# Optimization experiments

Measured on AMD Instinct MI355X. Metric: run time of the kernel, lower is better.

Reference implementation:

```python
import jax, jax.numpy as jnp
import numpy as np

B, I, M, R, C = 2048, 16, 4, 4096, 10  # batch, input_dim, num_mfs, num_rules, num_classes


def setup_inputs() -> dict:
    key = jax.random.key(0)
    k1, k2, k3, k4, k5 = jax.random.split(key, 5)
    x = jax.random.normal(k1, (B, I), dtype=jnp.float32)
    centers = jax.random.normal(k2, (I, M), dtype=jnp.float32)
    widths = jax.random.uniform(k3, (I, M), dtype=jnp.float32, minval=0.5, maxval=1.5)
    consequents = jax.random.normal(k4, (R, I + 1, C), dtype=jnp.float32)
    rule_idx = jax.random.randint(k5, (I, R), 0, M, dtype=jnp.int32)
    return {"x": x, "centers": centers, "widths": widths,
            "consequents": consequents, "rule_idx": rule_idx}


def reference(x, centers, widths, consequents, rule_idx):
    # Gaussian membership functions: [B, I, M] (note: +1e-9 inside exp, as in source)
    mfs = jnp.exp(-(x[:, :, None] - centers[None]) ** 2 / (2.0 * widths[None] ** 2) + 1e-9)
    # Gather per-rule MF values along the M axis: [B, I, R]
    rule_mfs = mfs[:, jnp.arange(I)[:, None], rule_idx]
    # Product t-norm over input dims -> firing strengths [B, R]
    firing = jnp.prod(rule_mfs, axis=1)
    norm_fs = firing / (jnp.sum(firing, axis=1, keepdims=True) + 1e-9)
    # Extended input with bias [B, I+1]
    x_ext = jnp.concatenate([x, jnp.ones((x.shape[0], 1), dtype=x.dtype)], axis=1)
    # Outer product phi [B, R, I+1], then flat GEMM with consequents
    phi = norm_fs[:, :, None] * jax.lax.stop_gradient(x_ext)[:, None, :]
    y_hat = phi.reshape(x.shape[0], R * (I + 1)) @ consequents.reshape(R * (I + 1), C)
    return y_hat, norm_fs, x_ext
```

## Files before the change

kernel.cpp:

```cpp
#include <hip/hip_runtime.h>
#include <stdint.h>

typedef short short8 __attribute__((ext_vector_type(8)));
typedef float f32x4 __attribute__((ext_vector_type(4)));

#define B_ 2048
#define I_ 16
#define M_ 4
#define R_ 4096
#define C_ 10
#define NX 17
#define NW 170
#define NPAD 192
#define KSPLIT 32
#define KCH (R_ / KSPLIT)

#define Y_OFF    0
#define NORM_OFF (B_ * C_)
#define XE_OFF   (B_ * C_ + B_ * R_)

#define PK_OFF    0
#define WT_OFF    16384
#define NFB_OFF   (WT_OFF + NPAD * R_ * 2)
#define PARTY_OFF (NFB_OFF + B_ * R_ * 2)

#define MFMA16(a, b, c) __builtin_amdgcn_mfma_f32_16x16x32_bf16(a, b, c, 0, 0, 0)

__device__ __forceinline__ uint16_t f2bf(float f) {
    uint32_t u = __builtin_bit_cast(uint32_t, f);
    uint32_t r = u + 0x7fffu + ((u >> 16) & 1u);
    return (uint16_t)(r >> 16);
}

__global__ __launch_bounds__(256) void prep_kernel(
        const int* __restrict__ rule_idx, const float* __restrict__ cons,
        uint32_t* __restrict__ packed, uint16_t* __restrict__ wt) {
    int t = threadIdx.x;
    if (blockIdx.x == 64) {
        for (int r = t; r < R_; r += 256) {
            uint32_t p = 0;
#pragma unroll
            for (int i = 0; i < I_; ++i)
                p |= ((uint32_t)rule_idx[i * R_ + r] & 3u) << (2 * i);
            packed[r] = p;
        }
        return;
    }
    __shared__ float lt[64][NW + 1];
    int k0 = blockIdx.x * 64;
    for (int idx = t; idx < 64 * NW; idx += 256) {
        int k = idx / NW, n = idx - k * NW;
        lt[k][n] = cons[(size_t)(k0 + k) * NW + n];
    }
    __syncthreads();
    for (int idx = t; idx < NPAD * 32; idx += 256) {
        int n = idx >> 5, kp = idx & 31;
        uint32_t v = 0;
        if (n < NW) {
            uint32_t v0 = f2bf(lt[kp * 2][n]);
            uint32_t v1 = f2bf(lt[kp * 2 + 1][n]);
            v = v0 | (v1 << 16);
        }
        *(uint32_t*)(wt + (size_t)n * R_ + k0 + kp * 2) = v;
    }
}

__global__ __launch_bounds__(256) void fuzz_kernel(
        const float* __restrict__ x, const float* __restrict__ centers,
        const float* __restrict__ widths, const uint32_t* __restrict__ packed,
        float* __restrict__ out, uint16_t* __restrict__ nfb) {
    int b = blockIdx.x;
    int t = threadIdx.x;
    __shared__ float xs[I_];
    __shared__ float zl[64];
    __shared__ float tab4[4 * 256];
    __shared__ float wsum[4];

    if (t < I_) xs[t] = x[b * I_ + t];
    if (t < NX) out[XE_OFF + b * NX + t] = (t < I_) ? x[b * I_ + t] : 1.0f;
    __syncthreads();

    if (t < 64) {
        int i = t >> 2, m = t & 3;
        float d = xs[i] - centers[i * M_ + m];
        float w = widths[i * M_ + m];
        zl[t] = -(d * d) / (2.0f * w * w) + 1e-9f;
    }
    __syncthreads();

#pragma unroll
    for (int u = 0; u < 4; ++u) {
        int idx = t + u * 256;
        int q = idx >> 8, xq = idx & 255;
        tab4[idx] = zl[q * 16 +      (xq & 3)]
                  + zl[q * 16 +  4 + ((xq >> 2) & 3)]
                  + zl[q * 16 +  8 + ((xq >> 4) & 3)]
                  + zl[q * 16 + 12 + ((xq >> 6) & 3)];
    }
    __syncthreads();

    float fs[16];
    float lsum = 0.f;
#pragma unroll
    for (int k = 0; k < 16; ++k) {
        uint32_t p = packed[t + k * 256];
        float s = tab4[        p         & 255]
                + tab4[256 + ((p >>  8) & 255)]
                + tab4[512 + ((p >> 16) & 255)]
                + tab4[768 + ((p >> 24) & 255)];
        float f = __expf(s);
        fs[k] = f;
        lsum += f;
    }
#pragma unroll
    for (int off = 32; off > 0; off >>= 1) lsum += __shfl_down(lsum, off);
    if ((t & 63) == 0) wsum[t >> 6] = lsum;
    __syncthreads();
    float inv = 1.0f / (wsum[0] + wsum[1] + wsum[2] + wsum[3] + 1e-9f);
#pragma unroll
    for (int k = 0; k < 16; ++k) {
        float v = fs[k] * inv;
        out[NORM_OFF + (size_t)b * R_ + t + k * 256] = v;
        nfb[(size_t)b * R_ + t + k * 256] = f2bf(v);
    }
}

__global__ __launch_bounds__(256, 3) void gemm_kernel(
        const uint16_t* __restrict__ nfb,
        const uint16_t* __restrict__ wt,
        const float* __restrict__ xe,
        float* __restrict__ party) {
    int bt  = blockIdx.x;
    int ks  = blockIdx.y;
    int tid = threadIdx.x;
    int wid = tid >> 6;
    int lane = tid & 63;
    int b0 = bt * 64;
    int k0 = ks * KCH;
    int row = lane & 15;
    int kf  = (lane >> 4) * 8;

    f32x4 acc[4][3];
#pragma unroll
    for (int mt = 0; mt < 4; ++mt)
#pragma unroll
        for (int nt = 0; nt < 3; ++nt) acc[mt][nt] = (f32x4){0.f, 0.f, 0.f, 0.f};

    const uint16_t* Ab = nfb + (size_t)(b0 + row) * R_ + k0 + kf;
    const uint16_t* Bb = wt  + (size_t)(wid * 48 + row) * R_ + k0 + kf;

    short8 a[2][4], w[2][3];
#define LOADS(buf, kk)                                                   \
    do {                                                                 \
        a[buf][0] = *(const short8*)(Ab + (kk));                         \
        a[buf][1] = *(const short8*)(Ab + (size_t)16 * R_ + (kk));       \
        a[buf][2] = *(const short8*)(Ab + (size_t)32 * R_ + (kk));       \
        a[buf][3] = *(const short8*)(Ab + (size_t)48 * R_ + (kk));       \
        w[buf][0] = *(const short8*)(Bb + (kk));                         \
        w[buf][1] = *(const short8*)(Bb + (size_t)16 * R_ + (kk));       \
        w[buf][2] = *(const short8*)(Bb + (size_t)32 * R_ + (kk));       \
    } while (0)

    LOADS(0, 0);
#pragma unroll
    for (int it = 0; it < KCH / 32; ++it) {
        int cur = it & 1;
        if (it + 1 < KCH / 32) LOADS(cur ^ 1, (it + 1) * 32);
#pragma unroll
        for (int nt = 0; nt < 3; ++nt)
#pragma unroll
            for (int mt = 0; mt < 4; ++mt)
                acc[mt][nt] = MFMA16(a[cur][mt], w[cur][nt], acc[mt][nt]);
    }
#undef LOADS

    __shared__ float tile[64][NPAD];
#pragma unroll
    for (int mt = 0; mt < 4; ++mt)
#pragma unroll
        for (int nt = 0; nt < 3; ++nt)
#pragma unroll
            for (int j = 0; j < 4; ++j)
                tile[mt * 16 + (lane >> 4) * 4 + j][wid * 48 + nt * 16 + row] =
                    acc[mt][nt][j];
    __syncthreads();

    for (int idx = tid; idx < 64 * C_; idx += 256) {
        int bl = idx / C_;
        int c  = idx - bl * C_;
        float y = tile[bl][I_ * C_ + c];
        const float* xrow = xe + (size_t)(b0 + bl) * NX;
#pragma unroll
        for (int j = 0; j < I_; ++j) y += xrow[j] * tile[bl][j * C_ + c];
        party[((size_t)ks * B_ + b0 + bl) * C_ + c] = y;
    }
}

__global__ __launch_bounds__(256) void finalize_kernel(
        const float* __restrict__ party, float* __restrict__ out) {
    int idx = blockIdx.x * 256 + threadIdx.x;
    if (idx < B_ * C_) {
        float s = 0.f;
#pragma unroll
        for (int ks = 0; ks < KSPLIT; ++ks) s += party[(size_t)ks * B_ * C_ + idx];
        out[Y_OFF + idx] = s;
    }
}

extern "C" void kernel_launch(void* const* d_in, const int* in_sizes, int n_in,
                              void* d_out, int out_size, void* d_ws, size_t ws_size,
                              hipStream_t stream) {
    const float* x       = (const float*)d_in[0];
    const float* centers = (const float*)d_in[1];
    const float* widths  = (const float*)d_in[2];
    const float* cons    = (const float*)d_in[3];
    const int*   ridx    = (const int*)d_in[4];
    float* out = (float*)d_out;

    uint32_t* packed = (uint32_t*)((char*)d_ws + PK_OFF);
    uint16_t* wt     = (uint16_t*)((char*)d_ws + WT_OFF);
    uint16_t* nfb    = (uint16_t*)((char*)d_ws + NFB_OFF);
    float*    party  = (float*)((char*)d_ws + PARTY_OFF);

    prep_kernel<<<dim3(65), dim3(256), 0, stream>>>(ridx, cons, packed, wt);
    fuzz_kernel<<<dim3(B_), dim3(256), 0, stream>>>(x, centers, widths, packed, out, nfb);
    gemm_kernel<<<dim3(B_ / 64, KSPLIT), dim3(256), 0, stream>>>(
        nfb, wt, out + XE_OFF, party);
    finalize_kernel<<<dim3((B_ * C_ + 255) / 256), dim3(256), 0, stream>>>(party, out);
}
```

Baseline: 47.12 us.

## Drop bf16 copy of normalized firing; GEMM reads fp32 output and converts in-register

The fuzz kernel no longer writes a separate bf16 copy of the normalized firing strengths. It assigns each thread 16 contiguous rules, so the packed rule indices are read and the fp32 output is written with vector accesses. The GEMM now reads the fp32 norm_fs directly from the output buffer and converts it to bf16 in registers before the MFMAs. This removes a 16 MB write and its workspace buffer, at the cost of doubling the A-operand read bytes in the GEMM and adding conversion instructions.

```diff
diff --git a/kernel.cpp b/kernel.cpp
--- a/kernel.cpp
+++ b/kernel.cpp
@@ -1,4 +1,5 @@
 #include <hip/hip_runtime.h>
+#include <hip/hip_bf16.h>
 #include <stdint.h>
 
 typedef short short8 __attribute__((ext_vector_type(8)));
@@ -14,6 +15,7 @@
 #define NPAD 192
 #define KSPLIT 32
 #define KCH (R_ / KSPLIT)
+#define NIT (KCH / 32)
 
 #define Y_OFF    0
 #define NORM_OFF (B_ * C_)
@@ -21,8 +23,7 @@
 
 #define PK_OFF    0
 #define WT_OFF    16384
-#define NFB_OFF   (WT_OFF + NPAD * R_ * 2)
-#define PARTY_OFF (NFB_OFF + B_ * R_ * 2)
+#define PARTY_OFF (WT_OFF + NPAD * R_ * 2)
 
 #define MFMA16(a, b, c) __builtin_amdgcn_mfma_f32_16x16x32_bf16(a, b, c, 0, 0, 0)
 
@@ -68,7 +69,7 @@
 __global__ __launch_bounds__(256) void fuzz_kernel(
         const float* __restrict__ x, const float* __restrict__ centers,
         const float* __restrict__ widths, const uint32_t* __restrict__ packed,
-        float* __restrict__ out, uint16_t* __restrict__ nfb) {
+        float* __restrict__ out) {
     int b = blockIdx.x;
     int t = threadIdx.x;
     __shared__ float xs[I_];
@@ -99,34 +100,45 @@
     }
     __syncthreads();
 
+    uint4 pk[4];
+#pragma unroll
+    for (int g = 0; g < 4; ++g)
+        pk[g] = *(const uint4*)(packed + t * 16 + g * 4);
+
     float fs[16];
     float lsum = 0.f;
 #pragma unroll
-    for (int k = 0; k < 16; ++k) {
-        uint32_t p = packed[t + k * 256];
-        float s = tab4[        p         & 255]
-                + tab4[256 + ((p >>  8) & 255)]
-                + tab4[512 + ((p >> 16) & 255)]
-                + tab4[768 + ((p >> 24) & 255)];
-        float f = __expf(s);
-        fs[k] = f;
-        lsum += f;
+    for (int g = 0; g < 4; ++g) {
+        const uint32_t pv[4] = {pk[g].x, pk[g].y, pk[g].z, pk[g].w};
+#pragma unroll
+        for (int j = 0; j < 4; ++j) {
+            uint32_t p = pv[j];
+            float s = tab4[        p         & 255]
+                    + tab4[256 + ((p >>  8) & 255)]
+                    + tab4[512 + ((p >> 16) & 255)]
+                    + tab4[768 + ((p >> 24) & 255)];
+            float f = __expf(s);
+            fs[g * 4 + j] = f;
+            lsum += f;
+        }
     }
 #pragma unroll
     for (int off = 32; off > 0; off >>= 1) lsum += __shfl_down(lsum, off);
     if ((t & 63) == 0) wsum[t >> 6] = lsum;
     __syncthreads();
     float inv = 1.0f / (wsum[0] + wsum[1] + wsum[2] + wsum[3] + 1e-9f);
-#pragma unroll
-    for (int k = 0; k < 16; ++k) {
-        float v = fs[k] * inv;
-        out[NORM_OFF + (size_t)b * R_ + t + k * 256] = v;
-        nfb[(size_t)b * R_ + t + k * 256] = f2bf(v);
+
+    float* orow = out + NORM_OFF + (size_t)b * R_ + t * 16;
+#pragma unroll
+    for (int u = 0; u < 4; ++u) {
+        f32x4 o = {fs[u * 4 + 0] * inv, fs[u * 4 + 1] * inv,
+                   fs[u * 4 + 2] * inv, fs[u * 4 + 3] * inv};
+        *(f32x4*)(orow + u * 4) = o;
     }
 }
 
 __global__ __launch_bounds__(256, 3) void gemm_kernel(
-        const uint16_t* __restrict__ nfb,
+        const float* __restrict__ nf,
         const uint16_t* __restrict__ wt,
         const float* __restrict__ xe,
         float* __restrict__ party) {
@@ -146,33 +158,60 @@
 #pragma unroll
         for (int nt = 0; nt < 3; ++nt) acc[mt][nt] = (f32x4){0.f, 0.f, 0.f, 0.f};
 
-    const uint16_t* Ab = nfb + (size_t)(b0 + row) * R_ + k0 + kf;
-    const uint16_t* Bb = wt  + (size_t)(wid * 48 + row) * R_ + k0 + kf;
-
-    short8 a[2][4], w[2][3];
-#define LOADS(buf, kk)                                                   \
+    const float*    Af = nf + (size_t)(b0 + row) * R_ + k0 + kf;
+    const uint16_t* Bb = wt + (size_t)(wid * 48 + row) * R_ + k0 + kf;
+
+    f32x4 fl[4], fh[4];
+    short8 abf[2][4], w[2][3];
+
+#define LOADF(kk)                                                        \
     do {                                                                 \
-        a[buf][0] = *(const short8*)(Ab + (kk));                         \
-        a[buf][1] = *(const short8*)(Ab + (size_t)16 * R_ + (kk));       \
-        a[buf][2] = *(const short8*)(Ab + (size_t)32 * R_ + (kk));       \
-        a[buf][3] = *(const short8*)(Ab + (size_t)48 * R_ + (kk));       \
+        _Pragma("unroll")                                                \
+        for (int r = 0; r < 4; ++r) {                                    \
+            fl[r] = *(const f32x4*)(Af + (size_t)(16 * r) * R_ + (kk));  \
+            fh[r] = *(const f32x4*)(Af + (size_t)(16 * r) * R_ + (kk) + 4); \
+        }                                                                \
+    } while (0)
+#define LOADW(buf, kk)                                                   \
+    do {                                                                 \
         w[buf][0] = *(const short8*)(Bb + (kk));                         \
         w[buf][1] = *(const short8*)(Bb + (size_t)16 * R_ + (kk));       \
         w[buf][2] = *(const short8*)(Bb + (size_t)32 * R_ + (kk));       \
     } while (0)
-
-    LOADS(0, 0);
-#pragma unroll
-    for (int it = 0; it < KCH / 32; ++it) {
+#define CVT(buf)                                                         \
+    do {                                                                 \
+        _Pragma("unroll")                                                \
+        for (int r = 0; r < 4; ++r) {                                    \
+            _Pragma("unroll")                                            \
+            for (int e = 0; e < 4; ++e) {                                \
+                abf[buf][r][e] = (short)__builtin_bit_cast(               \
+                    uint16_t, __float2bfloat16(fl[r][e]));                \
+                abf[buf][r][e + 4] = (short)__builtin_bit_cast(           \
+                    uint16_t, __float2bfloat16(fh[r][e]));                \
+            }                                                            \
+        }                                                                \
+    } while (0)
+
+    LOADF(0);
+    LOADW(0, 0);
+    CVT(0);
+#pragma unroll
+    for (int it = 0; it < NIT; ++it) {
         int cur = it & 1;
-        if (it + 1 < KCH / 32) LOADS(cur ^ 1, (it + 1) * 32);
+        if (it + 1 < NIT) {
+            LOADF((it + 1) * 32);
+            LOADW(cur ^ 1, (it + 1) * 32);
+        }
 #pragma unroll
         for (int nt = 0; nt < 3; ++nt)
 #pragma unroll
             for (int mt = 0; mt < 4; ++mt)
-                acc[mt][nt] = MFMA16(a[cur][mt], w[cur][nt], acc[mt][nt]);
-    }
-#undef LOADS
+                acc[mt][nt] = MFMA16(abf[cur][mt], w[cur][nt], acc[mt][nt]);
+        if (it + 1 < NIT) CVT(cur ^ 1);
+    }
+#undef LOADF
+#undef LOADW
+#undef CVT
 
     __shared__ float tile[64][NPAD];
 #pragma unroll
@@ -219,12 +258,11 @@
 
     uint32_t* packed = (uint32_t*)((char*)d_ws + PK_OFF);
     uint16_t* wt     = (uint16_t*)((char*)d_ws + WT_OFF);
-    uint16_t* nfb    = (uint16_t*)((char*)d_ws + NFB_OFF);
     float*    party  = (float*)((char*)d_ws + PARTY_OFF);
 
     prep_kernel<<<dim3(65), dim3(256), 0, stream>>>(ridx, cons, packed, wt);
-    fuzz_kernel<<<dim3(B_), dim3(256), 0, stream>>>(x, centers, widths, packed, out, nfb);
+    fuzz_kernel<<<dim3(B_), dim3(256), 0, stream>>>(x, centers, widths, packed, out);
     gemm_kernel<<<dim3(B_ / 64, KSPLIT), dim3(256), 0, stream>>>(
-        nfb, wt, out + XE_OFF, party);
+        out + NORM_OFF, wt, out + XE_OFF, party);
     finalize_kernel<<<dim3((B_ * C_ + 255) / 256), dim3(256), 0, stream>>>(party, out);
 }
```

Result: slower. 59.02 us (+25.2%).
